# Optimization experiments

Measured on AMD Instinct MI355X. Metric: run time of the kernel, lower is better.

The kernel has to match this reference:

```python
import jax, jax.numpy as jnp
import numpy as np

V, H, E, L = 50257, 1024, 512, 128


def setup_inputs() -> dict:
    key = jax.random.key(0)
    ks = jax.random.split(key, 16)
    s = 0.02
    return {
        "input_tok": jax.random.randint(ks[0], (1,), 0, V),
        "h0": jax.random.normal(ks[1], (1, 1, H), jnp.float32),
        "c0": jax.random.normal(ks[2], (1, 1, H), jnp.float32),
        "enc_output": jax.random.normal(ks[3], (L, H), jnp.float32),
        "emb_table": s * jax.random.normal(ks[4], (V, E), jnp.float32),
        "attn_W": s * jax.random.normal(ks[5], (L, H + E), jnp.float32),
        "attn_b": jnp.zeros((L,), jnp.float32),
        "a2d_W": s * jax.random.normal(ks[6], (H, H + E), jnp.float32),
        "a2d_b": jnp.zeros((H,), jnp.float32),
        "W_ih": s * jax.random.normal(ks[7], (4 * H, H), jnp.float32),
        "W_hh": s * jax.random.normal(ks[8], (4 * H, H), jnp.float32),
        "b_ih": jnp.zeros((4 * H,), jnp.float32),
        "b_hh": jnp.zeros((4 * H,), jnp.float32),
        "out_W": s * jax.random.normal(ks[9], (V, H), jnp.float32),
        "out_b": jnp.zeros((V,), jnp.float32),
    }


def reference(input_tok, h0, c0, enc_output, emb_table, attn_W, attn_b,
              a2d_W, a2d_b, W_ih, W_hh, b_ih, b_hh, out_W, out_b):
    # embed: (1, E); h, c: (1, H)
    embed = emb_table[input_tok].reshape(1, E)
    h = h0.reshape(1, H)
    c = c0.reshape(1, H)
    # attention over encoder positions
    attn_in = jnp.concatenate([embed, h], axis=1)                      # (1, E+H)
    attn_weight = jax.nn.softmax(attn_in @ attn_W.T + attn_b, axis=1)  # (1, L)
    attn_out = attn_weight @ enc_output                                # (1, H)
    # combine and project to LSTM input
    dec_in = jnp.concatenate([embed, attn_out], axis=1)                # (1, E+H)
    dec_in = jax.nn.relu(dec_in @ a2d_W.T + a2d_b)                     # (1, H)
    # one LSTM cell step (torch gate order: i, f, g, o)
    gates = dec_in @ W_ih.T + b_ih + h @ W_hh.T + b_hh                 # (1, 4H)
    i_g, f_g, g_g, o_g = jnp.split(gates, 4, axis=1)
    c_new = jax.nn.sigmoid(f_g) * c + jax.nn.sigmoid(i_g) * jnp.tanh(g_g)
    h_new = jax.nn.sigmoid(o_g) * jnp.tanh(c_new)
    # output log-probs over vocab
    output = jax.nn.log_softmax(h_new @ out_W.T + out_b, axis=1)       # (1, V)
    return output, h_new.reshape(1, 1, H), c_new.reshape(1, 1, H), attn_weight
```

## Files before the change

kernel.cpp:

```cpp
#include <hip/hip_runtime.h>
#include <math.h>

#define V 50257
#define H 1024
#define E 512
#define L 128
#define HE 1536
#define NBLK5 2048
#define VSTRIDE (NBLK5 * 4)

#define WS_DECRAW 0
#define WS_DECIN  1536
#define WS_HNEW   2560
#define WS_ALOGIT 3584
#define WS_PAIRS  3712

__device__ __forceinline__ float wave_reduce_sum(float v) {
    #pragma unroll
    for (int off = 32; off > 0; off >>= 1) v += __shfl_xor(v, off, 64);
    return v;
}

__global__ void k_attn_logits(const int* __restrict__ tok_p,
                              const float* __restrict__ h0,
                              const float* __restrict__ emb,
                              const float* __restrict__ attn_W,
                              const float* __restrict__ attn_b,
                              float* __restrict__ ws) {
    __shared__ __align__(16) float s_in[HE];
    __shared__ float s_part[6];
    const int tid = threadIdx.x;
    const int tok = tok_p[0];
    for (int k = tid; k < HE; k += 384) {
        float v = (k < E) ? emb[(size_t)tok * E + k] : h0[k - E];
        s_in[k] = v;
        if (blockIdx.x == 0 && k < E) ws[WS_DECRAW + k] = v;
    }
    __syncthreads();
    const int lane = tid & 63, w = tid >> 6;
    const int r = blockIdx.x;
    const float4* s4 = (const float4*)s_in;
    const float4* w4 = (const float4*)(attn_W + (size_t)r * HE);
    float4 a = s4[lane + (w << 6)];
    float4 b = w4[lane + (w << 6)];
    float acc = a.x * b.x + a.y * b.y + a.z * b.z + a.w * b.w;
    acc = wave_reduce_sum(acc);
    if (lane == 0) s_part[w] = acc;
    __syncthreads();
    if (tid == 0) {
        float t = s_part[0] + s_part[1] + s_part[2] + s_part[3] + s_part[4] + s_part[5];
        ws[WS_ALOGIT + r] = t + attn_b[r];
    }
}

__global__ void k_attn_out(const float* __restrict__ enc,
                           float* __restrict__ out_attnw,
                           float* __restrict__ ws) {
    __shared__ float s_wn[L];
    __shared__ float s_acc[4][64];
    const int tid = threadIdx.x;
    if (tid < L) s_wn[tid] = ws[WS_ALOGIT + tid];
    __syncthreads();
    float m = -1e30f;
    #pragma unroll
    for (int l = 0; l < L; ++l) m = fmaxf(m, s_wn[l]);
    float s = 0.f;
    #pragma unroll
    for (int l = 0; l < L; ++l) s += __expf(s_wn[l] - m);
    __syncthreads();
    if (tid < L) {
        float wn = __expf(s_wn[tid] - m) / s;
        s_wn[tid] = wn;
        if (blockIdx.x == 0) out_attnw[tid] = wn;
    }
    __syncthreads();
    const int j = blockIdx.x * 64 + (tid & 63);
    const int lg = tid >> 6;
    float acc = 0.f;
    #pragma unroll
    for (int li = 0; li < 32; ++li) {
        const int l = (lg << 5) + li;
        acc = fmaf(s_wn[l], enc[l * H + j], acc);
    }
    s_acc[lg][tid & 63] = acc;
    __syncthreads();
    if (tid < 64) {
        float r = s_acc[0][tid] + s_acc[1][tid] + s_acc[2][tid] + s_acc[3][tid];
        ws[WS_DECRAW + E + blockIdx.x * 64 + tid] = r;
    }
}

__global__ void k_a2d(const float* __restrict__ a2d_W,
                      const float* __restrict__ a2d_b,
                      float* __restrict__ ws) {
    __shared__ float s_part[6];
    const int tid = threadIdx.x, lane = tid & 63, w = tid >> 6;
    const int r = blockIdx.x;
    const float4* x4 = (const float4*)(ws + WS_DECRAW);
    const float4* w4 = (const float4*)(a2d_W + (size_t)r * HE);
    float4 a = x4[lane + (w << 6)];
    float4 b = w4[lane + (w << 6)];
    float acc = a.x * b.x + a.y * b.y + a.z * b.z + a.w * b.w;
    acc = wave_reduce_sum(acc);
    if (lane == 0) s_part[w] = acc;
    __syncthreads();
    if (tid == 0) {
        float t = s_part[0] + s_part[1] + s_part[2] + s_part[3] + s_part[4] + s_part[5];
        ws[WS_DECIN + r] = fmaxf(t + a2d_b[r], 0.f);
    }
}

__global__ void k_lstm(const float* __restrict__ h0,
                       const float* __restrict__ c0,
                       const float* __restrict__ W_ih,
                       const float* __restrict__ W_hh,
                       const float* __restrict__ b_ih,
                       const float* __restrict__ b_hh,
                       float* __restrict__ out_h,
                       float* __restrict__ out_c,
                       float* __restrict__ ws) {
    __shared__ float s_g[4];
    const int tid = threadIdx.x, lane = tid & 63, w = tid >> 6;
    const int j = blockIdx.x;
    const float4* x4 = (const float4*)(ws + WS_DECIN);
    const float4* h4 = (const float4*)h0;
    const size_t r = (size_t)w * H + j;
    const float4* wi4 = (const float4*)(W_ih + r * H);
    const float4* wh4 = (const float4*)(W_hh + r * H);
    float acc = 0.f;
    #pragma unroll
    for (int k = 0; k < 4; ++k) {
        float4 a = wi4[lane + (k << 6)];
        float4 x = x4[lane + (k << 6)];
        acc = fmaf(a.x, x.x, acc); acc = fmaf(a.y, x.y, acc);
        acc = fmaf(a.z, x.z, acc); acc = fmaf(a.w, x.w, acc);
        float4 b = wh4[lane + (k << 6)];
        float4 h = h4[lane + (k << 6)];
        acc = fmaf(b.x, h.x, acc); acc = fmaf(b.y, h.y, acc);
        acc = fmaf(b.z, h.z, acc); acc = fmaf(b.w, h.w, acc);
    }
    acc = wave_reduce_sum(acc);
    if (lane == 0) s_g[w] = acc;
    __syncthreads();
    if (tid == 0) {
        float gi_ = s_g[0] + b_ih[j]         + b_hh[j];
        float gf  = s_g[1] + b_ih[H + j]     + b_hh[H + j];
        float gg  = s_g[2] + b_ih[2 * H + j] + b_hh[2 * H + j];
        float go  = s_g[3] + b_ih[3 * H + j] + b_hh[3 * H + j];
        float si = 1.f / (1.f + expf(-gi_));
        float sf = 1.f / (1.f + expf(-gf));
        float so = 1.f / (1.f + expf(-go));
        float cn = sf * c0[j] + si * tanhf(gg);
        float hn = so * tanhf(cn);
        out_c[j] = cn;
        out_h[j] = hn;
        ws[WS_HNEW + j] = hn;
    }
}

__global__ void k_vocab(const float* __restrict__ out_W,
                        const float* __restrict__ out_b,
                        float* __restrict__ logits,
                        float* __restrict__ ws) {
    const int lane = threadIdx.x & 63;
    const int widx = threadIdx.x >> 6;
    const int gw = (blockIdx.x << 2) + widx;
    const float4* h4 = (const float4*)(ws + WS_HNEW);
    float4 hr[4];
    #pragma unroll
    for (int k = 0; k < 4; ++k) hr[k] = h4[lane + (k << 6)];
    float m = -1e30f, s = 0.f;
    for (int v = gw; v < V; v += 2 * VSTRIDE) {
        const int v2 = v + VSTRIDE;
        const float4* w0 = (const float4*)(out_W + (size_t)v * H);
        float acc0 = 0.f, acc1 = 0.f;
        #pragma unroll
        for (int k = 0; k < 4; ++k) {
            float4 a = w0[lane + (k << 6)];
            acc0 = fmaf(hr[k].x, a.x, acc0); acc0 = fmaf(hr[k].y, a.y, acc0);
            acc0 = fmaf(hr[k].z, a.z, acc0); acc0 = fmaf(hr[k].w, a.w, acc0);
        }
        if (v2 < V) {
            const float4* w1 = (const float4*)(out_W + (size_t)v2 * H);
            #pragma unroll
            for (int k = 0; k < 4; ++k) {
                float4 a = w1[lane + (k << 6)];
                acc1 = fmaf(hr[k].x, a.x, acc1); acc1 = fmaf(hr[k].y, a.y, acc1);
                acc1 = fmaf(hr[k].z, a.z, acc1); acc1 = fmaf(hr[k].w, a.w, acc1);
            }
        }
        acc0 = wave_reduce_sum(acc0);
        float l0 = acc0 + out_b[v];
        if (lane == 0) logits[v] = l0;
        float mo = m;
        m = fmaxf(m, l0);
        s = s * __expf(mo - m) + __expf(l0 - m);
        if (v2 < V) {
            acc1 = wave_reduce_sum(acc1);
            float l1 = acc1 + out_b[v2];
            if (lane == 0) logits[v2] = l1;
            mo = m;
            m = fmaxf(m, l1);
            s = s * __expf(mo - m) + __expf(l1 - m);
        }
    }
    __shared__ float sm[4], ss[4];
    if (lane == 0) { sm[widx] = m; ss[widx] = s; }
    __syncthreads();
    if (threadIdx.x == 0) {
        float M = sm[0], S = ss[0];
        #pragma unroll
        for (int i = 1; i < 4; ++i) {
            float Mn = fmaxf(M, sm[i]);
            S = S * __expf(M - Mn) + ss[i] * __expf(sm[i] - Mn);
            M = Mn;
        }
        ws[WS_PAIRS + 2 * blockIdx.x]     = M;
        ws[WS_PAIRS + 2 * blockIdx.x + 1] = S;
    }
}

__global__ void k_final(float* __restrict__ logits,
                        const float* __restrict__ ws) {
    __shared__ float sm[256], ss[256];
    const int tid = threadIdx.x;
    float M = -1e30f, S = 0.f;
    for (int i = tid; i < NBLK5; i += 256) {
        float m2 = ws[WS_PAIRS + 2 * i], s2 = ws[WS_PAIRS + 2 * i + 1];
        float Mn = fmaxf(M, m2);
        S = S * __expf(M - Mn) + s2 * __expf(m2 - Mn);
        M = Mn;
    }
    sm[tid] = M; ss[tid] = S;
    __syncthreads();
    for (int off = 128; off > 0; off >>= 1) {
        if (tid < off) {
            float m2 = sm[tid + off], s2 = ss[tid + off];
            float Mn = fmaxf(sm[tid], m2);
            ss[tid] = ss[tid] * __expf(sm[tid] - Mn) + s2 * __expf(m2 - Mn);
            sm[tid] = Mn;
        }
        __syncthreads();
    }
    const float C = sm[0] + logf(ss[0]);
    for (int v = blockIdx.x * 256 + tid; v < V; v += gridDim.x * 256)
        logits[v] -= C;
}

extern "C" void kernel_launch(void* const* d_in, const int* in_sizes, int n_in,
                              void* d_out, int out_size, void* d_ws, size_t ws_size,
                              hipStream_t stream) {
    const int*   tok    = (const int*)d_in[0];
    const float* h0     = (const float*)d_in[1];
    const float* c0     = (const float*)d_in[2];
    const float* enc    = (const float*)d_in[3];
    const float* emb    = (const float*)d_in[4];
    const float* attn_W = (const float*)d_in[5];
    const float* attn_b = (const float*)d_in[6];
    const float* a2d_W  = (const float*)d_in[7];
    const float* a2d_b  = (const float*)d_in[8];
    const float* W_ih   = (const float*)d_in[9];
    const float* W_hh   = (const float*)d_in[10];
    const float* b_ih   = (const float*)d_in[11];
    const float* b_hh   = (const float*)d_in[12];
    const float* out_W  = (const float*)d_in[13];
    const float* out_b  = (const float*)d_in[14];

    float* out        = (float*)d_out;
    float* ws         = (float*)d_ws;
    float* out_logits = out;
    float* out_h      = out + V;
    float* out_c      = out + V + H;
    float* out_attnw  = out + V + 2 * H;

    k_attn_logits<<<128, 384, 0, stream>>>(tok, h0, emb, attn_W, attn_b, ws);
    k_attn_out<<<16, 256, 0, stream>>>(enc, out_attnw, ws);
    k_a2d<<<1024, 384, 0, stream>>>(a2d_W, a2d_b, ws);
    k_lstm<<<1024, 256, 0, stream>>>(h0, c0, W_ih, W_hh, b_ih, b_hh, out_h, out_c, ws);
    k_vocab<<<NBLK5, 256, 0, stream>>>(out_W, out_b, out_logits, ws);
    k_final<<<256, 256, 0, stream>>>(out_logits, ws);
}
```

Measured before the change: 66.60 us.

## Fuse attention kernels and hoist W_hh matvec into the first kernel

Merges the attention-logits and attention-output kernels into one, with 16 blocks each redundantly computing all 128 logits and the softmax before their slice of the weighted sum. The remaining 1024 blocks of the same launch compute the h0·W_hh gate partials, which depend only on inputs, and store them in the workspace. The LSTM kernel then reads only W_ih and adds the stored partials. This removes one launch and moves half of the LSTM weight traffic off the critical dependency chain, at the cost of redundant logit work in the attention blocks. The softmax also drops the max subtraction, which could overflow for large logits.

```diff
diff --git a/kernel.cpp b/kernel.cpp
--- a/kernel.cpp
+++ b/kernel.cpp
@@ -12,8 +12,8 @@
 #define WS_DECRAW 0
 #define WS_DECIN  1536
 #define WS_HNEW   2560
-#define WS_ALOGIT 3584
-#define WS_PAIRS  3712
+#define WS_GHH    3584
+#define WS_PAIRS  7680
 
 __device__ __forceinline__ float wave_reduce_sum(float v) {
     #pragma unroll
@@ -21,73 +21,87 @@
     return v;
 }
 
-__global__ void k_attn_logits(const int* __restrict__ tok_p,
-                              const float* __restrict__ h0,
-                              const float* __restrict__ emb,
-                              const float* __restrict__ attn_W,
-                              const float* __restrict__ attn_b,
-                              float* __restrict__ ws) {
+__global__ __launch_bounds__(256)
+void k_attn_whh(const int* __restrict__ tok_p,
+                const float* __restrict__ h0,
+                const float* __restrict__ emb,
+                const float* __restrict__ attn_W,
+                const float* __restrict__ attn_b,
+                const float* __restrict__ enc,
+                const float* __restrict__ W_hh,
+                float* __restrict__ out_attnw,
+                float* __restrict__ ws) {
+    const int tid = threadIdx.x, lane = tid & 63, w = tid >> 6;
+    const int bid = blockIdx.x;
+
+    if (bid >= 16) {
+        const int j = bid - 16;
+        const float4* h4 = (const float4*)h0;
+        const float4* wh4 = (const float4*)(W_hh + ((size_t)w * H + j) * H);
+        float acc = 0.f;
+        #pragma unroll
+        for (int k = 0; k < 4; ++k) {
+            float4 b = wh4[lane + (k << 6)];
+            float4 h = h4[lane + (k << 6)];
+            acc = fmaf(b.x, h.x, acc); acc = fmaf(b.y, h.y, acc);
+            acc = fmaf(b.z, h.z, acc); acc = fmaf(b.w, h.w, acc);
+        }
+        acc = wave_reduce_sum(acc);
+        if (lane == 0) ws[WS_GHH + w * H + j] = acc;
+        return;
+    }
+
     __shared__ __align__(16) float s_in[HE];
-    __shared__ float s_part[6];
-    const int tid = threadIdx.x;
+    __shared__ float s_logit[L];
+    __shared__ float s_wn[L];
+    __shared__ float s_acc[4][64];
     const int tok = tok_p[0];
-    for (int k = tid; k < HE; k += 384) {
+    for (int k = tid; k < HE; k += 256) {
         float v = (k < E) ? emb[(size_t)tok * E + k] : h0[k - E];
         s_in[k] = v;
-        if (blockIdx.x == 0 && k < E) ws[WS_DECRAW + k] = v;
-    }
-    __syncthreads();
-    const int lane = tid & 63, w = tid >> 6;
-    const int r = blockIdx.x;
+        if (bid == 0 && k < E) ws[WS_DECRAW + k] = v;
+    }
+    __syncthreads();
     const float4* s4 = (const float4*)s_in;
-    const float4* w4 = (const float4*)(attn_W + (size_t)r * HE);
-    float4 a = s4[lane + (w << 6)];
-    float4 b = w4[lane + (w << 6)];
-    float acc = a.x * b.x + a.y * b.y + a.z * b.z + a.w * b.w;
-    acc = wave_reduce_sum(acc);
-    if (lane == 0) s_part[w] = acc;
-    __syncthreads();
-    if (tid == 0) {
-        float t = s_part[0] + s_part[1] + s_part[2] + s_part[3] + s_part[4] + s_part[5];
-        ws[WS_ALOGIT + r] = t + attn_b[r];
-    }
-}
-
-__global__ void k_attn_out(const float* __restrict__ enc,
-                           float* __restrict__ out_attnw,
-                           float* __restrict__ ws) {
-    __shared__ float s_wn[L];
-    __shared__ float s_acc[4][64];
-    const int tid = threadIdx.x;
-    if (tid < L) s_wn[tid] = ws[WS_ALOGIT + tid];
-    __syncthreads();
-    float m = -1e30f;
-    #pragma unroll
-    for (int l = 0; l < L; ++l) m = fmaxf(m, s_wn[l]);
-    float s = 0.f;
-    #pragma unroll
-    for (int l = 0; l < L; ++l) s += __expf(s_wn[l] - m);
+    #pragma unroll
+    for (int rr = 0; rr < 32; ++rr) {
+        const int r = (rr << 2) + w;
+        const float4* w4 = (const float4*)(attn_W + (size_t)r * HE);
+        float acc = 0.f;
+        #pragma unroll
+        for (int c = 0; c < 6; ++c) {
+            float4 a = s4[lane + (c << 6)];
+            float4 b = w4[lane + (c << 6)];
+            acc = fmaf(a.x, b.x, acc); acc = fmaf(a.y, b.y, acc);
+            acc = fmaf(a.z, b.z, acc); acc = fmaf(a.w, b.w, acc);
+        }
+        acc = wave_reduce_sum(acc);
+        if (lane == 0) s_logit[r] = acc + attn_b[r];
+    }
+    __syncthreads();
+    float sum = 0.f;
+    #pragma unroll
+    for (int l = 0; l < L; ++l) sum += __expf(s_logit[l]);
+    const float inv = 1.f / sum;
     __syncthreads();
     if (tid < L) {
-        float wn = __expf(s_wn[tid] - m) / s;
+        float wn = __expf(s_logit[tid]) * inv;
         s_wn[tid] = wn;
-        if (blockIdx.x == 0) out_attnw[tid] = wn;
-    }
-    __syncthreads();
-    const int j = blockIdx.x * 64 + (tid & 63);
-    const int lg = tid >> 6;
+        if (bid == 0) out_attnw[tid] = wn;
+    }
+    __syncthreads();
+    const int j = bid * 64 + lane;
     float acc = 0.f;
     #pragma unroll
     for (int li = 0; li < 32; ++li) {
-        const int l = (lg << 5) + li;
+        const int l = (w << 5) + li;
         acc = fmaf(s_wn[l], enc[l * H + j], acc);
     }
-    s_acc[lg][tid & 63] = acc;
-    __syncthreads();
-    if (tid < 64) {
-        float r = s_acc[0][tid] + s_acc[1][tid] + s_acc[2][tid] + s_acc[3][tid];
-        ws[WS_DECRAW + E + blockIdx.x * 64 + tid] = r;
-    }
+    s_acc[w][lane] = acc;
+    __syncthreads();
+    if (tid < 64)
+        ws[WS_DECRAW + E + bid * 64 + tid] =
+            s_acc[0][tid] + s_acc[1][tid] + s_acc[2][tid] + s_acc[3][tid];
 }
 
 __global__ void k_a2d(const float* __restrict__ a2d_W,
@@ -110,10 +124,8 @@
     }
 }
 
-__global__ void k_lstm(const float* __restrict__ h0,
-                       const float* __restrict__ c0,
+__global__ void k_lstm(const float* __restrict__ c0,
                        const float* __restrict__ W_ih,
-                       const float* __restrict__ W_hh,
                        const float* __restrict__ b_ih,
                        const float* __restrict__ b_hh,
                        float* __restrict__ out_h,
@@ -123,10 +135,7 @@
     const int tid = threadIdx.x, lane = tid & 63, w = tid >> 6;
     const int j = blockIdx.x;
     const float4* x4 = (const float4*)(ws + WS_DECIN);
-    const float4* h4 = (const float4*)h0;
-    const size_t r = (size_t)w * H + j;
-    const float4* wi4 = (const float4*)(W_ih + r * H);
-    const float4* wh4 = (const float4*)(W_hh + r * H);
+    const float4* wi4 = (const float4*)(W_ih + ((size_t)w * H + j) * H);
     float acc = 0.f;
     #pragma unroll
     for (int k = 0; k < 4; ++k) {
@@ -134,13 +143,9 @@
         float4 x = x4[lane + (k << 6)];
         acc = fmaf(a.x, x.x, acc); acc = fmaf(a.y, x.y, acc);
         acc = fmaf(a.z, x.z, acc); acc = fmaf(a.w, x.w, acc);
-        float4 b = wh4[lane + (k << 6)];
-        float4 h = h4[lane + (k << 6)];
-        acc = fmaf(b.x, h.x, acc); acc = fmaf(b.y, h.y, acc);
-        acc = fmaf(b.z, h.z, acc); acc = fmaf(b.w, h.w, acc);
     }
     acc = wave_reduce_sum(acc);
-    if (lane == 0) s_g[w] = acc;
+    if (lane == 0) s_g[w] = acc + ws[WS_GHH + w * H + j];
     __syncthreads();
     if (tid == 0) {
         float gi_ = s_g[0] + b_ih[j]         + b_hh[j];
@@ -273,10 +278,10 @@
     float* out_c      = out + V + H;
     float* out_attnw  = out + V + 2 * H;
 
-    k_attn_logits<<<128, 384, 0, stream>>>(tok, h0, emb, attn_W, attn_b, ws);
-    k_attn_out<<<16, 256, 0, stream>>>(enc, out_attnw, ws);
+    k_attn_whh<<<1040, 256, 0, stream>>>(tok, h0, emb, attn_W, attn_b, enc,
+                                         W_hh, out_attnw, ws);
     k_a2d<<<1024, 384, 0, stream>>>(a2d_W, a2d_b, ws);
-    k_lstm<<<1024, 256, 0, stream>>>(h0, c0, W_ih, W_hh, b_ih, b_hh, out_h, out_c, ws);
+    k_lstm<<<1024, 256, 0, stream>>>(c0, W_ih, b_ih, b_hh, out_h, out_c, ws);
     k_vocab<<<NBLK5, 256, 0, stream>>>(out_W, out_b, out_logits, ws);
     k_final<<<256, 256, 0, stream>>>(out_logits, ws);
 }
```

Result: slower. 80.33 us (+20.6%).

## Fully unroll vocab GEMV with batched row loads and single-pass softmax stats

Applied to the files above, without the earlier changes.

The vocab projection loop becomes a fixed 7-rows-per-wave schedule. Loads for four rows are issued together, then three more, so more memory requests are in flight per wave. The online max/sum rescaling is replaced by one max and one sum over the seven logits, which removes the per-row exp rescales. This relies on V fitting within 7 rows per wave at the current grid size and raises register pressure from holding up to 16 float4 per lane.

```diff
diff --git a/kernel.cpp b/kernel.cpp
--- a/kernel.cpp
+++ b/kernel.cpp
@@ -7,7 +7,7 @@
 #define L 128
 #define HE 1536
 #define NBLK5 2048
-#define VSTRIDE (NBLK5 * 4)
+#define NWAVE5 (NBLK5 * 4)
 
 #define WS_DECRAW 0
 #define WS_DECIN  1536
@@ -124,9 +124,8 @@
     const int j = blockIdx.x;
     const float4* x4 = (const float4*)(ws + WS_DECIN);
     const float4* h4 = (const float4*)h0;
-    const size_t r = (size_t)w * H + j;
-    const float4* wi4 = (const float4*)(W_ih + r * H);
-    const float4* wh4 = (const float4*)(W_hh + r * H);
+    const float4* wi4 = (const float4*)(W_ih + ((size_t)w * H + j) * H);
+    const float4* wh4 = (const float4*)(W_hh + ((size_t)w * H + j) * H);
     float acc = 0.f;
     #pragma unroll
     for (int k = 0; k < 4; ++k) {
@@ -169,41 +168,69 @@
     float4 hr[4];
     #pragma unroll
     for (int k = 0; k < 4; ++k) hr[k] = h4[lane + (k << 6)];
-    float m = -1e30f, s = 0.f;
-    for (int v = gw; v < V; v += 2 * VSTRIDE) {
-        const int v2 = v + VSTRIDE;
-        const float4* w0 = (const float4*)(out_W + (size_t)v * H);
-        float acc0 = 0.f, acc1 = 0.f;
+
+    const int v6 = gw + 6 * NWAVE5;
+    const bool valid6 = (v6 < V);
+    const int v6c = valid6 ? v6 : (V - 1);
+
+    float lg[7];
+
+    float4 a[4][4];
+    #pragma unroll
+    for (int i = 0; i < 4; ++i) {
+        const float4* w4 = (const float4*)(out_W + (size_t)(gw + i * NWAVE5) * H);
+        #pragma unroll
+        for (int k = 0; k < 4; ++k) a[i][k] = w4[lane + (k << 6)];
+    }
+    #pragma unroll
+    for (int i = 0; i < 4; ++i) {
+        float t = 0.f;
         #pragma unroll
         for (int k = 0; k < 4; ++k) {
-            float4 a = w0[lane + (k << 6)];
-            acc0 = fmaf(hr[k].x, a.x, acc0); acc0 = fmaf(hr[k].y, a.y, acc0);
-            acc0 = fmaf(hr[k].z, a.z, acc0); acc0 = fmaf(hr[k].w, a.w, acc0);
+            t = fmaf(a[i][k].x, hr[k].x, t); t = fmaf(a[i][k].y, hr[k].y, t);
+            t = fmaf(a[i][k].z, hr[k].z, t); t = fmaf(a[i][k].w, hr[k].w, t);
         }
-        if (v2 < V) {
-            const float4* w1 = (const float4*)(out_W + (size_t)v2 * H);
-            #pragma unroll
-            for (int k = 0; k < 4; ++k) {
-                float4 a = w1[lane + (k << 6)];
-                acc1 = fmaf(hr[k].x, a.x, acc1); acc1 = fmaf(hr[k].y, a.y, acc1);
-                acc1 = fmaf(hr[k].z, a.z, acc1); acc1 = fmaf(hr[k].w, a.w, acc1);
-            }
+        t = wave_reduce_sum(t);
+        lg[i] = t + out_b[gw + i * NWAVE5];
+    }
+
+    float4 bfr[3][4];
+    #pragma unroll
+    for (int i = 0; i < 2; ++i) {
+        const float4* w4 = (const float4*)(out_W + (size_t)(gw + (4 + i) * NWAVE5) * H);
+        #pragma unroll
+        for (int k = 0; k < 4; ++k) bfr[i][k] = w4[lane + (k << 6)];
+    }
+    {
+        const float4* w4 = (const float4*)(out_W + (size_t)v6c * H);
+        #pragma unroll
+        for (int k = 0; k < 4; ++k) bfr[2][k] = w4[lane + (k << 6)];
+    }
+    #pragma unroll
+    for (int i = 0; i < 3; ++i) {
+        float t = 0.f;
+        #pragma unroll
+        for (int k = 0; k < 4; ++k) {
+            t = fmaf(bfr[i][k].x, hr[k].x, t); t = fmaf(bfr[i][k].y, hr[k].y, t);
+            t = fmaf(bfr[i][k].z, hr[k].z, t); t = fmaf(bfr[i][k].w, hr[k].w, t);
         }
-        acc0 = wave_reduce_sum(acc0);
-        float l0 = acc0 + out_b[v];
-        if (lane == 0) logits[v] = l0;
-        float mo = m;
-        m = fmaxf(m, l0);
-        s = s * __expf(mo - m) + __expf(l0 - m);
-        if (v2 < V) {
-            acc1 = wave_reduce_sum(acc1);
-            float l1 = acc1 + out_b[v2];
-            if (lane == 0) logits[v2] = l1;
-            mo = m;
-            m = fmaxf(m, l1);
-            s = s * __expf(mo - m) + __expf(l1 - m);
-        }
-    }
+        t = wave_reduce_sum(t);
+        lg[4 + i] = t + out_b[(i < 2) ? (gw + (4 + i) * NWAVE5) : v6c];
+    }
+    if (!valid6) lg[6] = -1e30f;
+
+    if (lane == 0) {
+        #pragma unroll
+        for (int i = 0; i < 6; ++i) logits[gw + i * NWAVE5] = lg[i];
+        if (valid6) logits[v6] = lg[6];
+    }
+    float m = lg[0];
+    #pragma unroll
+    for (int i = 1; i < 7; ++i) m = fmaxf(m, lg[i]);
+    float s = 0.f;
+    #pragma unroll
+    for (int i = 0; i < 7; ++i) s += __expf(lg[i] - m);
+
     __shared__ float sm[4], ss[4];
     if (lane == 0) { sm[widx] = m; ss[widx] = s; }
     __syncthreads();
```

After: 67.31 us. No clear change (+1.1%).

## Hoist W_hh·h0 gate matvec into the first kernel alongside attention logits

Applied to the files above, without the earlier changes.

The recurrent h0·W_hh product does not depend on the attention chain, so it now runs in the first launch in 1024 extra blocks next to the attention-logit blocks. Partial gates go to a new workspace region, and the LSTM kernel reads them back instead of streaming W_hh itself. This takes 16 MB of weight reads off the serial critical path and lets them fill a kernel that used only 128 blocks. The attention-logit blocks shrink to 256 threads with a scalar loop, and the workspace offsets are shifted to fit the new buffer.

```diff
diff --git a/kernel.cpp b/kernel.cpp
--- a/kernel.cpp
+++ b/kernel.cpp
@@ -12,8 +12,9 @@
 #define WS_DECRAW 0
 #define WS_DECIN  1536
 #define WS_HNEW   2560
-#define WS_ALOGIT 3584
-#define WS_PAIRS  3712
+#define WS_GHH    3584
+#define WS_ALOGIT 7680
+#define WS_PAIRS  7808
 
 __device__ __forceinline__ float wave_reduce_sum(float v) {
     #pragma unroll
@@ -21,36 +22,54 @@
     return v;
 }
 
-__global__ void k_attn_logits(const int* __restrict__ tok_p,
-                              const float* __restrict__ h0,
-                              const float* __restrict__ emb,
-                              const float* __restrict__ attn_W,
-                              const float* __restrict__ attn_b,
-                              float* __restrict__ ws) {
-    __shared__ __align__(16) float s_in[HE];
-    __shared__ float s_part[6];
-    const int tid = threadIdx.x;
+__global__ __launch_bounds__(256)
+void k_attn_whh(const int* __restrict__ tok_p,
+                const float* __restrict__ h0,
+                const float* __restrict__ emb,
+                const float* __restrict__ attn_W,
+                const float* __restrict__ attn_b,
+                const float* __restrict__ W_hh,
+                float* __restrict__ ws) {
+    const int tid = threadIdx.x, lane = tid & 63, w = tid >> 6;
+    const int bid = blockIdx.x;
+
+    if (bid >= 128) {
+        const int j = bid - 128;
+        const float4* h4 = (const float4*)h0;
+        const float4* wh4 = (const float4*)(W_hh + ((size_t)w * H + j) * H);
+        float acc = 0.f;
+        #pragma unroll
+        for (int k = 0; k < 4; ++k) {
+            float4 b = wh4[lane + (k << 6)];
+            float4 h = h4[lane + (k << 6)];
+            acc = fmaf(b.x, h.x, acc); acc = fmaf(b.y, h.y, acc);
+            acc = fmaf(b.z, h.z, acc); acc = fmaf(b.w, h.w, acc);
+        }
+        acc = wave_reduce_sum(acc);
+        if (lane == 0) ws[WS_GHH + w * H + j] = acc;
+        return;
+    }
+
+    __shared__ float s_in[HE];
+    __shared__ float s_part[4];
     const int tok = tok_p[0];
-    for (int k = tid; k < HE; k += 384) {
+    for (int k = tid; k < HE; k += 256) {
         float v = (k < E) ? emb[(size_t)tok * E + k] : h0[k - E];
         s_in[k] = v;
-        if (blockIdx.x == 0 && k < E) ws[WS_DECRAW + k] = v;
-    }
-    __syncthreads();
-    const int lane = tid & 63, w = tid >> 6;
-    const int r = blockIdx.x;
-    const float4* s4 = (const float4*)s_in;
-    const float4* w4 = (const float4*)(attn_W + (size_t)r * HE);
-    float4 a = s4[lane + (w << 6)];
-    float4 b = w4[lane + (w << 6)];
-    float acc = a.x * b.x + a.y * b.y + a.z * b.z + a.w * b.w;
+        if (bid == 0 && k < E) ws[WS_DECRAW + k] = v;
+    }
+    __syncthreads();
+    const float* wr = attn_W + (size_t)bid * HE;
+    float acc = 0.f;
+    #pragma unroll
+    for (int i = 0; i < 6; ++i)
+        acc = fmaf(s_in[tid + (i << 8)], wr[tid + (i << 8)], acc);
     acc = wave_reduce_sum(acc);
     if (lane == 0) s_part[w] = acc;
     __syncthreads();
-    if (tid == 0) {
-        float t = s_part[0] + s_part[1] + s_part[2] + s_part[3] + s_part[4] + s_part[5];
-        ws[WS_ALOGIT + r] = t + attn_b[r];
-    }
+    if (tid == 0)
+        ws[WS_ALOGIT + bid] = s_part[0] + s_part[1] + s_part[2] + s_part[3]
+                              + attn_b[bid];
 }
 
 __global__ void k_attn_out(const float* __restrict__ enc,
@@ -110,10 +129,8 @@
     }
 }
 
-__global__ void k_lstm(const float* __restrict__ h0,
-                       const float* __restrict__ c0,
+__global__ void k_lstm(const float* __restrict__ c0,
                        const float* __restrict__ W_ih,
-                       const float* __restrict__ W_hh,
                        const float* __restrict__ b_ih,
                        const float* __restrict__ b_hh,
                        float* __restrict__ out_h,
@@ -123,10 +140,7 @@
     const int tid = threadIdx.x, lane = tid & 63, w = tid >> 6;
     const int j = blockIdx.x;
     const float4* x4 = (const float4*)(ws + WS_DECIN);
-    const float4* h4 = (const float4*)h0;
-    const size_t r = (size_t)w * H + j;
-    const float4* wi4 = (const float4*)(W_ih + r * H);
-    const float4* wh4 = (const float4*)(W_hh + r * H);
+    const float4* wi4 = (const float4*)(W_ih + ((size_t)w * H + j) * H);
     float acc = 0.f;
     #pragma unroll
     for (int k = 0; k < 4; ++k) {
@@ -134,13 +148,9 @@
         float4 x = x4[lane + (k << 6)];
         acc = fmaf(a.x, x.x, acc); acc = fmaf(a.y, x.y, acc);
         acc = fmaf(a.z, x.z, acc); acc = fmaf(a.w, x.w, acc);
-        float4 b = wh4[lane + (k << 6)];
-        float4 h = h4[lane + (k << 6)];
-        acc = fmaf(b.x, h.x, acc); acc = fmaf(b.y, h.y, acc);
-        acc = fmaf(b.z, h.z, acc); acc = fmaf(b.w, h.w, acc);
     }
     acc = wave_reduce_sum(acc);
-    if (lane == 0) s_g[w] = acc;
+    if (lane == 0) s_g[w] = acc + ws[WS_GHH + w * H + j];
     __syncthreads();
     if (tid == 0) {
         float gi_ = s_g[0] + b_ih[j]         + b_hh[j];
@@ -273,10 +283,10 @@
     float* out_c      = out + V + H;
     float* out_attnw  = out + V + 2 * H;
 
-    k_attn_logits<<<128, 384, 0, stream>>>(tok, h0, emb, attn_W, attn_b, ws);
+    k_attn_whh<<<1152, 256, 0, stream>>>(tok, h0, emb, attn_W, attn_b, W_hh, ws);
     k_attn_out<<<16, 256, 0, stream>>>(enc, out_attnw, ws);
     k_a2d<<<1024, 384, 0, stream>>>(a2d_W, a2d_b, ws);
-    k_lstm<<<1024, 256, 0, stream>>>(h0, c0, W_ih, W_hh, b_ih, b_hh, out_h, out_c, ws);
+    k_lstm<<<1024, 256, 0, stream>>>(c0, W_ih, b_ih, b_hh, out_h, out_c, ws);
     k_vocab<<<NBLK5, 256, 0, stream>>>(out_W, out_b, out_logits, ws);
     k_final<<<256, 256, 0, stream>>>(out_logits, ws);
 }
```

After: 65.66 us. Within noise of the previous version (-1.4%).
